# Kernel optimization log

Measured on AMD Instinct MI355X. Metric: run time of the kernel, lower is better.

The kernel has to match this reference:

```python
import jax, jax.numpy as jnp
import numpy as np

B, T, N_IN, N_RES, N_OUT = 64, 512, 2000, 50, 500
SPECTRAL_RADIUS = 0.7


def setup_inputs() -> dict:
    key = jax.random.key(0)
    k_x, k_in, k_res, k_ker, k_b = jax.random.split(key, 5)
    inputs = jax.random.normal(k_x, (B, T, N_IN), dtype=jnp.float32)
    W_in = jax.random.uniform(k_in, (N_RES, N_IN), minval=-0.5, maxval=0.5, dtype=jnp.float32)
    W_res_raw = np.asarray(jax.random.uniform(k_res, (N_RES, N_RES), minval=-0.5, maxval=0.5, dtype=jnp.float32))
    # spectral-radius normalization (host-side eig, matches tf.linalg.eigvals scaling)
    rho = np.max(np.abs(np.linalg.eigvals(W_res_raw.astype(np.float64))))
    W_res = jnp.asarray((W_res_raw / rho * SPECTRAL_RADIUS).astype(np.float32))
    # Dense(n_outputs, tanh): glorot-uniform kernel, zero bias
    lim = np.sqrt(6.0 / (N_RES + N_OUT))
    W_out_kernel = jax.random.uniform(k_ker, (N_RES, N_OUT), minval=-lim, maxval=lim, dtype=jnp.float32)
    W_out_bias = jnp.zeros((N_OUT,), dtype=jnp.float32)
    return {"inputs": inputs, "W_in": W_in, "W_res": W_res,
            "W_out_kernel": W_out_kernel, "W_out_bias": W_out_bias}


def reference(inputs, W_in, W_res, W_out_kernel, W_out_bias):
    # inputs: [B, T, n_in]; recurrence: state = tanh(tanh(u) @ W_in^T + state @ W_res^T)
    batch = inputs.shape[0]
    state0 = jnp.zeros((batch, W_in.shape[0]), dtype=inputs.dtype)

    def step(state, u_t):  # u_t: [B, n_in]
        u = jnp.tanh(u_t)
        new_state = jnp.tanh(u @ W_in.T + state @ W_res.T)
        return new_state, None

    final_state, _ = jax.lax.scan(step, state0, jnp.swapaxes(inputs, 0, 1))
    # readout uses only the last state: Dense(tanh)
    return jnp.tanh(final_state @ W_out_kernel + W_out_bias)
```

## Files before the change

kernel.cpp:

```cpp
#include <hip/hip_runtime.h>
#include <cstdint>

#define NIN     2000
#define NRES    50
#define NOUT    500
#define TSTEPS  512
#define NBATCH  64
#define BT      32768
#define KPAD    2048
#define NPAD    64
#define KSTEPS  63
#define KCLAMP  1996

typedef __bf16 bf16x8 __attribute__((ext_vector_type(8)));
typedef float  f32x4  __attribute__((ext_vector_type(4)));

__device__ __forceinline__ float fast_tanh(float x) {
  float e = __expf(2.0f * x);
  return fmaf(-2.0f, __builtin_amdgcn_rcpf(e + 1.0f), 1.0f);
}

__device__ __forceinline__ void bf16_split(float x, unsigned short& h, unsigned short& l) {
  unsigned u  = __float_as_uint(x);
  unsigned hb = (u + 0x7FFFu + ((u >> 16) & 1u)) & 0xFFFF0000u;
  h = (unsigned short)(hb >> 16);
  float lo = x - __uint_as_float(hb);
  l = (unsigned short)(__float_as_uint(lo) >> 16);
}

union ABfrag { unsigned short u16[8]; bf16x8 v; };

__global__ __launch_bounds__(256) void prep_kernel(const float* __restrict__ Win,
                                                   unsigned short* __restrict__ Whi,
                                                   unsigned short* __restrict__ Wlo) {
  int idx = blockIdx.x * 256 + threadIdx.x;
  int n = idx >> 11;
  int k = idx & (KPAD - 1);
  float x = (n < NRES && k < NIN) ? Win[n * NIN + k] : 0.0f;
  unsigned short h, l;
  bf16_split(x, h, l);
  Whi[idx] = h;
  Wlo[idx] = l;
}

__global__ __launch_bounds__(256) void proj_mfma(const float* __restrict__ U,
                                                 const unsigned short* __restrict__ Whi,
                                                 const unsigned short* __restrict__ Wlo,
                                                 float* __restrict__ P) {
  const int wave = threadIdx.x >> 6;
  const int lane = threadIdx.x & 63;
  const int mrow = lane & 15;
  const int g    = lane >> 4;
  const int g8   = g * 8;
  const int row0 = (blockIdx.x * 4 + wave) * 16;

  const float* __restrict__ u = U + (size_t)(row0 + mrow) * NIN;

  const unsigned short* bhp[4];
  const unsigned short* blp[4];
#pragma unroll
  for (int f = 0; f < 4; ++f) {
    const int n = f * 16 + mrow;
    bhp[f] = Whi + n * KPAD + g8;
    blp[f] = Wlo + n * KPAD + g8;
  }

  f32x4 acc[4] = {};

  float4 ca = *(const float4*)(u + min(g8, KCLAMP));
  float4 cb = *(const float4*)(u + min(g8 + 4, KCLAMP));

  for (int s = 0; s < KSTEPS; ++s) {
    const int k0 = s * 32;
    const int kn = k0 + 32;
    float4 na = *(const float4*)(u + min(kn + g8, KCLAMP));
    float4 nb = *(const float4*)(u + min(kn + g8 + 4, KCLAMP));

    bf16x8 bh[4], bl[4];
#pragma unroll
    for (int f = 0; f < 4; ++f) {
      bh[f] = *(const bf16x8*)(bhp[f] + k0);
      bl[f] = *(const bf16x8*)(blp[f] + k0);
    }

    float t[8];
    t[0] = fast_tanh(ca.x); t[1] = fast_tanh(ca.y);
    t[2] = fast_tanh(ca.z); t[3] = fast_tanh(ca.w);
    t[4] = fast_tanh(cb.x); t[5] = fast_tanh(cb.y);
    t[6] = fast_tanh(cb.z); t[7] = fast_tanh(cb.w);

    ABfrag ah, al;
#pragma unroll
    for (int j = 0; j < 8; ++j) bf16_split(t[j], ah.u16[j], al.u16[j]);

#pragma unroll
    for (int f = 0; f < 4; ++f)
      acc[f] = __builtin_amdgcn_mfma_f32_16x16x32_bf16(ah.v, bh[f], acc[f], 0, 0, 0);
#pragma unroll
    for (int f = 0; f < 4; ++f)
      acc[f] = __builtin_amdgcn_mfma_f32_16x16x32_bf16(al.v, bh[f], acc[f], 0, 0, 0);
#pragma unroll
    for (int f = 0; f < 4; ++f)
      acc[f] = __builtin_amdgcn_mfma_f32_16x16x32_bf16(ah.v, bl[f], acc[f], 0, 0, 0);

    ca = na; cb = nb;
  }

#pragma unroll
  for (int f = 0; f < 4; ++f) {
    const int col = f * 16 + mrow;
    if (col < NRES) {
#pragma unroll
      for (int i = 0; i < 4; ++i) {
        const int r = row0 + g * 4 + i;
        P[(size_t)r * NRES + col] = acc[f][i];
      }
    }
  }
}

__global__ __launch_bounds__(64, 1) void recur_kernel(const float* __restrict__ P,
                                                      const float* __restrict__ W_res,
                                                      const float* __restrict__ W_out,
                                                      const float* __restrict__ bias,
                                                      float* __restrict__ out) {
  __shared__ float sbuf[64];
  const int b    = blockIdx.x;
  const int lane = threadIdx.x;
  const int r    = (lane < NRES) ? lane : 0;

  float w[52];
#pragma unroll
  for (int j = 0; j < NRES; ++j) w[j] = W_res[r * NRES + j];
  w[50] = 0.0f; w[51] = 0.0f;

  const float* Pb = P + (size_t)b * TSTEPS * NRES;
  float state = 0.0f;

  float pring[16];
#pragma unroll
  for (int i = 0; i < 16; ++i) pring[i] = Pb[i * NRES + r];

#pragma unroll 16
  for (int t = 0; t < TSTEPS; ++t) {
    float pcur = pring[t & 15];
    pring[t & 15] = Pb[(t + 16) * NRES + r];

    sbuf[lane] = state;
    __syncthreads();

    float a0 = pcur, a1 = 0.0f, a2 = 0.0f, a3 = 0.0f;
    float a4 = 0.0f, a5 = 0.0f, a6 = 0.0f, a7 = 0.0f;
#pragma unroll
    for (int q = 0; q < 12; q += 2) {
      float4 sA = *(const float4*)&sbuf[q * 4];
      float4 sB = *(const float4*)&sbuf[q * 4 + 4];
      a0 = fmaf(sA.x, w[4 * q + 0], a0);
      a1 = fmaf(sA.y, w[4 * q + 1], a1);
      a2 = fmaf(sA.z, w[4 * q + 2], a2);
      a3 = fmaf(sA.w, w[4 * q + 3], a3);
      a4 = fmaf(sB.x, w[4 * q + 4], a4);
      a5 = fmaf(sB.y, w[4 * q + 5], a5);
      a6 = fmaf(sB.z, w[4 * q + 6], a6);
      a7 = fmaf(sB.w, w[4 * q + 7], a7);
    }
    {
      float4 sA = *(const float4*)&sbuf[48];
      a0 = fmaf(sA.x, w[48], a0);
      a1 = fmaf(sA.y, w[49], a1);
      a2 = fmaf(sA.z, w[50], a2);
      a3 = fmaf(sA.w, w[51], a3);
    }
    state = fast_tanh(((a0 + a1) + (a2 + a3)) + ((a4 + a5) + (a6 + a7)));
  }

  sbuf[lane] = state;
  __syncthreads();

#pragma unroll
  for (int kk = 0; kk < 8; ++kk) {
    int o = kk * 64 + lane;
    if (o < NOUT) {
      float a0 = bias[o];
      float a1 = 0.0f;
#pragma unroll
      for (int q = 0; q < 12; ++q) {
        float4 s4 = *(const float4*)&sbuf[q * 4];
        a0 = fmaf(s4.x, W_out[(4 * q + 0) * NOUT + o], a0);
        a1 = fmaf(s4.y, W_out[(4 * q + 1) * NOUT + o], a1);
        a0 = fmaf(s4.z, W_out[(4 * q + 2) * NOUT + o], a0);
        a1 = fmaf(s4.w, W_out[(4 * q + 3) * NOUT + o], a1);
      }
      {
        float4 s4 = *(const float4*)&sbuf[48];
        a0 = fmaf(s4.x, W_out[48 * NOUT + o], a0);
        a1 = fmaf(s4.y, W_out[49 * NOUT + o], a1);
      }
      out[b * NOUT + o] = fast_tanh(a0 + a1);
    }
  }
}

extern "C" void kernel_launch(void* const* d_in, const int* in_sizes, int n_in,
                              void* d_out, int out_size, void* d_ws, size_t ws_size,
                              hipStream_t stream) {
  const float* inputs = (const float*)d_in[0];
  const float* W_in   = (const float*)d_in[1];
  const float* W_res  = (const float*)d_in[2];
  const float* W_out  = (const float*)d_in[3];
  const float* bias   = (const float*)d_in[4];
  float* out = (float*)d_out;

  float* P = (float*)d_ws;
  unsigned short* Whi = (unsigned short*)((char*)d_ws + (size_t)BT * NRES * 4);
  unsigned short* Wlo = Whi + NPAD * KPAD;

  prep_kernel<<<(NPAD * KPAD) / 256, 256, 0, stream>>>(W_in, Whi, Wlo);
  proj_mfma<<<BT / 64, 256, 0, stream>>>(inputs, Whi, Wlo, P);
  recur_kernel<<<NBATCH, 64, 0, stream>>>(P, W_res, W_out, bias, out);
}
```

Baseline: 583.4 us.

## Stage repacked W_in fragments in double-buffered LDS shared across waves

The prep kernel now writes W_in's bf16 hi/lo split directly in MFMA fragment order. The projection kernel cooperatively loads each K-step's B fragments into a double-buffered LDS tile that all four waves share, so each wave no longer fetches its own copy from global or cache. This cuts redundant B-operand traffic but adds a block-wide barrier every K-step. Separately, the single-wave recurrence kernel swaps __syncthreads for a wave barrier to make each serial step cheaper.

```diff
diff --git a/kernel.cpp b/kernel.cpp
--- a/kernel.cpp
+++ b/kernel.cpp
@@ -7,9 +7,8 @@
 #define TSTEPS  512
 #define NBATCH  64
 #define BT      32768
-#define KPAD    2048
-#define NPAD    64
 #define KSTEPS  63
+#define SPAD    64
 #define KCLAMP  1996
 
 typedef __bf16 bf16x8 __attribute__((ext_vector_type(8)));
@@ -31,22 +30,31 @@
 union ABfrag { unsigned short u16[8]; bf16x8 v; };
 
 __global__ __launch_bounds__(256) void prep_kernel(const float* __restrict__ Win,
-                                                   unsigned short* __restrict__ Whi,
-                                                   unsigned short* __restrict__ Wlo) {
-  int idx = blockIdx.x * 256 + threadIdx.x;
-  int n = idx >> 11;
-  int k = idx & (KPAD - 1);
-  float x = (n < NRES && k < NIN) ? Win[n * NIN + k] : 0.0f;
-  unsigned short h, l;
-  bf16_split(x, h, l);
-  Whi[idx] = h;
-  Wlo[idx] = l;
-}
-
-__global__ __launch_bounds__(256) void proj_mfma(const float* __restrict__ U,
-                                                 const unsigned short* __restrict__ Whi,
-                                                 const unsigned short* __restrict__ Wlo,
-                                                 float* __restrict__ P) {
+                                                   unsigned short* __restrict__ Bpk) {
+  int tid  = blockIdx.x * 256 + threadIdx.x;
+  int l    = tid & 63;
+  int rest = tid >> 6;
+  int f    = rest & 3;
+  int p    = (rest >> 2) & 1;
+  int s    = rest >> 3;
+  int n    = f * 16 + (l & 15);
+  int kb   = s * 32 + (l >> 4) * 8;
+  unsigned short v[8];
+#pragma unroll
+  for (int j = 0; j < 8; ++j) {
+    int k = kb + j;
+    float x = (n < NRES && k < NIN) ? Win[n * NIN + k] : 0.0f;
+    unsigned short h, lo;
+    bf16_split(x, h, lo);
+    v[j] = p ? lo : h;
+  }
+  *reinterpret_cast<uint4*>(Bpk + (size_t)tid * 8) = *reinterpret_cast<uint4*>(v);
+}
+
+__global__ __launch_bounds__(256, 2) void proj_mfma(const float* __restrict__ U,
+                                                    const unsigned short* __restrict__ Bpk,
+                                                    float* __restrict__ P) {
+  __shared__ __align__(16) unsigned short lds[2][4096];
   const int wave = threadIdx.x >> 6;
   const int lane = threadIdx.x & 63;
   const int mrow = lane & 15;
@@ -56,31 +64,38 @@
 
   const float* __restrict__ u = U + (size_t)(row0 + mrow) * NIN;
 
-  const unsigned short* bhp[4];
-  const unsigned short* blp[4];
-#pragma unroll
-  for (int f = 0; f < 4; ++f) {
-    const int n = f * 16 + mrow;
-    bhp[f] = Whi + n * KPAD + g8;
-    blp[f] = Wlo + n * KPAD + g8;
-  }
+  const int c0 = wave * 2, c1 = c0 + 1;
+  const unsigned short* src0 = Bpk + ((size_t)c0 * 64 + lane) * 8;
+  const unsigned short* src1 = Bpk + ((size_t)c1 * 64 + lane) * 8;
+  unsigned short* dst0[2] = { &lds[0][(c0 * 64 + lane) * 8], &lds[1][(c0 * 64 + lane) * 8] };
+  unsigned short* dst1[2] = { &lds[0][(c1 * 64 + lane) * 8], &lds[1][(c1 * 64 + lane) * 8] };
 
   f32x4 acc[4] = {};
 
+  {
+    uint4 s0 = *reinterpret_cast<const uint4*>(src0);
+    uint4 s1 = *reinterpret_cast<const uint4*>(src1);
+    *reinterpret_cast<uint4*>(dst0[0]) = s0;
+    *reinterpret_cast<uint4*>(dst1[0]) = s1;
+  }
   float4 ca = *(const float4*)(u + min(g8, KCLAMP));
   float4 cb = *(const float4*)(u + min(g8 + 4, KCLAMP));
+  __syncthreads();
 
   for (int s = 0; s < KSTEPS; ++s) {
-    const int k0 = s * 32;
-    const int kn = k0 + 32;
+    const int cur = s & 1, nxt = cur ^ 1;
+    const int kn = s * 32 + 32;
+
+    uint4 n0 = *reinterpret_cast<const uint4*>(src0 + (size_t)(s + 1) * 4096);
+    uint4 n1 = *reinterpret_cast<const uint4*>(src1 + (size_t)(s + 1) * 4096);
     float4 na = *(const float4*)(u + min(kn + g8, KCLAMP));
     float4 nb = *(const float4*)(u + min(kn + g8 + 4, KCLAMP));
 
     bf16x8 bh[4], bl[4];
 #pragma unroll
     for (int f = 0; f < 4; ++f) {
-      bh[f] = *(const bf16x8*)(bhp[f] + k0);
-      bl[f] = *(const bf16x8*)(blp[f] + k0);
+      bh[f] = *(const bf16x8*)&lds[cur][(f * 64 + lane) * 8];
+      bl[f] = *(const bf16x8*)&lds[cur][((4 + f) * 64 + lane) * 8];
     }
 
     float t[8];
@@ -102,6 +117,10 @@
 #pragma unroll
     for (int f = 0; f < 4; ++f)
       acc[f] = __builtin_amdgcn_mfma_f32_16x16x32_bf16(ah.v, bl[f], acc[f], 0, 0, 0);
+
+    *reinterpret_cast<uint4*>(dst0[nxt]) = n0;
+    *reinterpret_cast<uint4*>(dst1[nxt]) = n1;
+    __syncthreads();
 
     ca = na; cb = nb;
   }
@@ -147,7 +166,7 @@
     pring[t & 15] = Pb[(t + 16) * NRES + r];
 
     sbuf[lane] = state;
-    __syncthreads();
+    __builtin_amdgcn_wave_barrier();
 
     float a0 = pcur, a1 = 0.0f, a2 = 0.0f, a3 = 0.0f;
     float a4 = 0.0f, a5 = 0.0f, a6 = 0.0f, a7 = 0.0f;
@@ -175,7 +194,7 @@
   }
 
   sbuf[lane] = state;
-  __syncthreads();
+  __builtin_amdgcn_wave_barrier();
 
 #pragma unroll
   for (int kk = 0; kk < 8; ++kk) {
@@ -212,10 +231,9 @@
   float* out = (float*)d_out;
 
   float* P = (float*)d_ws;
-  unsigned short* Whi = (unsigned short*)((char*)d_ws + (size_t)BT * NRES * 4);
-  unsigned short* Wlo = Whi + NPAD * KPAD;
-
-  prep_kernel<<<(NPAD * KPAD) / 256, 256, 0, stream>>>(W_in, Whi, Wlo);
-  proj_mfma<<<BT / 64, 256, 0, stream>>>(inputs, Whi, Wlo, P);
+  unsigned short* Bpk = (unsigned short*)((char*)d_ws + (size_t)BT * NRES * 4);
+
+  prep_kernel<<<128, 256, 0, stream>>>(W_in, Bpk);
+  proj_mfma<<<BT / 64, 256, 0, stream>>>(inputs, Bpk, P);
   recur_kernel<<<NBATCH, 64, 0, stream>>>(P, W_res, W_out, bias, out);
 }
```

After: 569.8 us. -2.3%, faster.
